# Optimization experiments

Measured on AMD Instinct MI355X. Metric: run time of the kernel, lower is better.

## Reference

```python
import jax, jax.numpy as jnp
import numpy as np

N_NODES = 50000
N_EDGES = 800000
D_FEAT = 100


def setup_inputs() -> dict:
    key = jax.random.key(0)
    ks = jax.random.split(key, 10)
    s = 0.1
    x = jax.random.normal(ks[0], (N_NODES, D_FEAT), dtype=jnp.float32)
    edge_index = jax.random.randint(ks[1], (2, N_EDGES), 0, N_NODES, dtype=jnp.int32)
    return {
        "x": x,
        "edge_index": edge_index,
        "convW0": jax.random.normal(ks[2], (100, 100), jnp.float32) * s,
        "convb0": jnp.zeros((100,), jnp.float32),
        "convW1": jax.random.normal(ks[3], (100, 100), jnp.float32) * s,
        "convb1": jnp.zeros((100,), jnp.float32),
        "linW0": jax.random.normal(ks[4], (100, 10), jnp.float32) * s,
        "linb0": jnp.zeros((10,), jnp.float32),
        "linW1": jax.random.normal(ks[5], (10, 1), jnp.float32) * s,
        "linb1": jnp.zeros((1,), jnp.float32),
    }


def _gcn_conv(x, W, b, src, dst, n):
    """PyG GCNConv: h = x @ W; out[i] = sum_{(j->i)} d_j^{-1/2} d_i^{-1/2} h[j] + b,
    with self-loops already included in (src, dst)."""
    h = x @ W  # [N, out]
    deg = jax.ops.segment_sum(jnp.ones(src.shape[0], x.dtype), dst, num_segments=n)
    dinv = jnp.where(deg > 0, jax.lax.rsqrt(deg), jnp.zeros_like(deg))
    norm = dinv[src] * dinv[dst]  # [E_tot]
    msg = norm[:, None] * h[src]  # gather [E_tot, out]
    out = jax.ops.segment_sum(msg, dst, num_segments=n)  # scatter-add
    return out + b


def reference(x, edge_index, convW0, convb0, convW1, convb1, linW0, linb0, linW1, linb1):
    n = x.shape[0]
    # global-norm division (x.div(torch.norm(x).detach()))
    nm = jax.lax.stop_gradient(jnp.linalg.norm(x))
    x = x / nm
    # NOTE: original re-assigns x via sklearn SelectKBest(chi2, k=100) on raw data.x;
    # that is non-differentiable data preprocessing, so we assume x already holds the
    # k=100 selected features.
    loops = jnp.arange(n, dtype=edge_index.dtype)
    src = jnp.concatenate([edge_index[0], loops])  # self-loops appended
    dst = jnp.concatenate([edge_index[1], loops])
    x = _gcn_conv(x, convW0, convb0, src, dst, n)
    x = _gcn_conv(x, convW1, convb1, src, dst, n)
    # MLP head: ReLU between layers, no activation after the last (loop breaks)
    x = jax.nn.relu(x @ linW0 + linb0)
    x = x @ linW1 + linb1
    return x.T  # [1, N]
```

## Files before the change

### kernel.cpp

```cpp
#include <hip/hip_runtime.h>

#define NN 50000
#define DF 100
#define NE 800000

__device__ __forceinline__ int xcc_id() {
    int x;
    asm volatile("s_getreg_b32 %0, hwreg(HW_REG_XCC_ID)" : "=s"(x));
    return x & 7;
}

__device__ __forceinline__ float wredf(float v) {
    #pragma unroll
    for (int o = 32; o > 0; o >>= 1) v += __shfl_down(v, o, 64);
    return v;
}

__global__ __launch_bounds__(256) void k_pre(const float* __restrict__ x,
                                             float* __restrict__ acc,
                                             const int* __restrict__ src,
                                             const int* __restrict__ dst,
                                             int* __restrict__ cur,
                                             int* __restrict__ ell,
                                             const float* __restrict__ W0,
                                             const float* __restrict__ W1,
                                             const float* __restrict__ cb0,
                                             const float* __restrict__ cb1,
                                             const float* __restrict__ L0,
                                             const float* __restrict__ lb0,
                                             float* __restrict__ Wz,
                                             float* __restrict__ uvec,
                                             float* __restrict__ cvec) {
    int b = blockIdx.x, t = threadIdx.x;
    if (b < 3125) {
        int e = b * 256 + t;
        int d = dst[e];
        int g = xcc_id();
        int p = __hip_atomic_fetch_add(&cur[g * NN + d], 1, __ATOMIC_RELAXED,
                                       __HIP_MEMORY_SCOPE_WORKGROUP);
        if (p < 16) ell[d * 128 + g * 16 + p] = src[e];
    } else if (b < 4149) {
        const float4* x4 = (const float4*)x;
        const int n4 = NN * DF / 4;
        int tid = (b - 3125) * 256 + t, stride = 1024 * 256;
        float s = 0.f;
        for (int i = tid; i < n4; i += stride) {
            float4 v = x4[i];
            s += v.x * v.x + v.y * v.y + v.z * v.z + v.w * v.w;
        }
        s = wredf(s);
        __shared__ float p[4];
        int lane = t & 63, w = t >> 6;
        if (lane == 0) p[w] = s;
        __syncthreads();
        if (t == 0) atomicAdd(acc, p[0] + p[1] + p[2] + p[3]);
    } else {
        __shared__ float WA[1000];
        for (int o = t; o < 1000; o += 256) {
            int j = o / 10, m = o % 10;
            float s = 0.f;
            for (int k = 0; k < 100; ++k) s += W1[j * 100 + k] * L0[k * 10 + m];
            WA[o] = s;
        }
        __syncthreads();
        for (int o = t; o < 1000; o += 256) {
            int i = o / 10, m = o % 10;
            float s = 0.f;
            for (int k = 0; k < 100; ++k) s += W0[i * 100 + k] * WA[k * 10 + m];
            Wz[o] = s;
        }
        if (t < 10) {
            float su = 0.f, scv = 0.f;
            for (int k = 0; k < 100; ++k) {
                su  += cb0[k] * WA[k * 10 + t];
                scv += cb1[k] * L0[k * 10 + t];
            }
            uvec[t] = su;
            cvec[t] = scv + lb0[t];
        }
    }
}

__global__ __launch_bounds__(256) void k_ygemm(const float* __restrict__ x,
                                               const float* __restrict__ Wz,
                                               const int* __restrict__ cur,
                                               int* __restrict__ ell,
                                               int* __restrict__ cnt4A,
                                               float* __restrict__ dinvA,
                                               float* __restrict__ gp) {
    __shared__ float w[1000];
    for (int o = threadIdx.x; o < 1000; o += 256) w[o] = Wz[o];
    __syncthreads();
    int i = blockIdx.x * 256 + threadIdx.x;
    if (i > NN) return;
    if (i == NN) {
        float4 z = {0.f, 0.f, 0.f, 0.f};
        float4* d4 = (float4*)(gp + NN * 16);
        d4[0] = z; d4[1] = z; d4[2] = z; d4[3] = z;
        return;
    }
    int* rp = ell + i * 128;
    int c0 = min(cur[i], 16);
    int total = c0;
    int wpos = c0;
    for (int r = 1; r < 8; ++r) {
        int cr = min(cur[r * NN + i], 16);
        total += cr;
        for (int j = 0; j < cr; ++j) rp[wpos + j] = rp[r * 16 + j];
        wpos += cr;
    }
    int cnt4 = (total + 3) & ~3;
    for (int j = total; j < cnt4; ++j) rp[j] = NN;
    cnt4A[i] = cnt4;
    float dv = rsqrtf((float)(total + 1));
    dinvA[i] = dv;

    const float4* r4 = (const float4*)(x + i * 100);
    float h[10];
    #pragma unroll
    for (int m = 0; m < 10; ++m) h[m] = 0.f;
    for (int kk = 0; kk < 25; ++kk) {
        float4 a = r4[kk];
        #pragma unroll
        for (int j = 0; j < 4; ++j) {
            float av = ((const float*)&a)[j];
            int k = kk * 4 + j;
            #pragma unroll
            for (int m = 0; m < 10; ++m) h[m] += av * w[k * 10 + m];
        }
    }
    float o16[16];
    #pragma unroll
    for (int m = 0; m < 10; ++m) o16[m] = dv * h[m];
    o16[10] = dv;
    o16[11] = o16[12] = o16[13] = o16[14] = o16[15] = 0.f;
    float4* dst4 = (float4*)(gp + i * 16);
    #pragma unroll
    for (int q = 0; q < 4; ++q) dst4[q] = *(float4*)&o16[q * 4];
}

__global__ __launch_bounds__(256) void k_agg1(const float* __restrict__ gp,
                                              const int* __restrict__ cnt4A,
                                              const float* __restrict__ dinvA,
                                              const int* __restrict__ ell,
                                              const float* __restrict__ sumsq,
                                              float* __restrict__ tb) {
    int n = (blockIdx.x * 256 + threadIdx.x) >> 6;
    int l = threadIdx.x & 63;
    int g = l >> 4, lane16 = l & 15;
    if (n > NN) return;
    if (n == NN) {
        if (l < 16) tb[NN * 16 + lane16] = 0.f;
        return;
    }
    int cnt4 = cnt4A[n];
    const int* rp = ell + n * 128;
    float a0 = (g == 0) ? gp[n * 16 + lane16] : 0.f;
    float a1 = 0.f, a2 = 0.f, a3 = 0.f;
    int J = cnt4 >> 2, k = g;
    for (; J >= 4; J -= 4, k += 16) {
        int i0 = rp[k], i1 = rp[k + 4], i2 = rp[k + 8], i3 = rp[k + 12];
        a0 += gp[i0 * 16 + lane16];
        a1 += gp[i1 * 16 + lane16];
        a2 += gp[i2 * 16 + lane16];
        a3 += gp[i3 * 16 + lane16];
    }
    for (; J > 0; --J, k += 4) a0 += gp[rp[k] * 16 + lane16];
    float acc = (a0 + a1) + (a2 + a3);
    acc += __shfl_xor(acc, 16, 64);
    acc += __shfl_xor(acc, 32, 64);
    if (l < 16) {
        float dv = dinvA[n];
        float sc = rsqrtf(*sumsq);
        float o = (lane16 < 10) ? sc * dv * dv * acc
                                : (lane16 == 10 ? dv * acc : 0.f);
        tb[n * 16 + lane16] = o;
    }
}

__global__ __launch_bounds__(256) void k_agg2(const float* __restrict__ tb,
                                              const int* __restrict__ cnt4A,
                                              const float* __restrict__ dinvA,
                                              const int* __restrict__ ell,
                                              const float* __restrict__ u,
                                              const float* __restrict__ cvec,
                                              const float* __restrict__ L1,
                                              const float* __restrict__ lb1,
                                              float* __restrict__ out) {
    __shared__ float su[10], scv[10], sl[10];
    if (threadIdx.x < 10) {
        su[threadIdx.x] = u[threadIdx.x];
        scv[threadIdx.x] = cvec[threadIdx.x];
        sl[threadIdx.x] = L1[threadIdx.x];
    }
    __syncthreads();
    int n = (blockIdx.x * 256 + threadIdx.x) >> 6;
    int l = threadIdx.x & 63;
    int g = l >> 4, lane16 = l & 15;
    int cnt4 = cnt4A[n];
    const int* rp = ell + n * 128;
    float a0 = (g == 0) ? tb[n * 16 + lane16] : 0.f;
    float a1 = 0.f, a2 = 0.f, a3 = 0.f;
    int J = cnt4 >> 2, k = g;
    for (; J >= 4; J -= 4, k += 16) {
        int i0 = rp[k], i1 = rp[k + 4], i2 = rp[k + 8], i3 = rp[k + 12];
        a0 += tb[i0 * 16 + lane16];
        a1 += tb[i1 * 16 + lane16];
        a2 += tb[i2 * 16 + lane16];
        a3 += tb[i3 * 16 + lane16];
    }
    for (; J > 0; --J, k += 4) a0 += tb[rp[k] * 16 + lane16];
    float acc = (a0 + a1) + (a2 + a3);
    acc += __shfl_xor(acc, 16, 64);
    acc += __shfl_xor(acc, 32, 64);
    if (l < 16) {
        float dv = dinvA[n];
        float v = tb[n * 16 + 10];
        float hidden = 0.f;
        if (lane16 < 10)
            hidden = fmaxf(dv * acc + v * su[lane16] + scv[lane16], 0.f) * sl[lane16];
        #pragma unroll
        for (int o = 8; o; o >>= 1) hidden += __shfl_down(hidden, o, 16);
        if (lane16 == 0) out[n] = hidden + lb1[0];
    }
}

extern "C" void kernel_launch(void* const* d_in, const int* in_sizes, int n_in,
                              void* d_out, int out_size, void* d_ws, size_t ws_size,
                              hipStream_t stream) {
    const float* x   = (const float*)d_in[0];
    const int*   ei  = (const int*)d_in[1];
    const int*   src = ei;
    const int*   dst = ei + NE;
    const float* W0  = (const float*)d_in[2];
    const float* cb0 = (const float*)d_in[3];
    const float* W1  = (const float*)d_in[4];
    const float* cb1 = (const float*)d_in[5];
    const float* lw0 = (const float*)d_in[6];
    const float* lb0 = (const float*)d_in[7];
    const float* lw1 = (const float*)d_in[8];
    const float* lb1 = (const float*)d_in[9];
    float* out = (float*)d_out;

    char* ws = (char*)d_ws;
    float* acc     = (float*)(ws + 0);
    int*   cur     = (int*)  (ws + 256);
    const size_t zspan = 1600256;
    float* Wz      = (float*)(ws + 1600512);
    float* uvec    = (float*)(ws + 1604608);
    float* cvec    = (float*)(ws + 1604736);
    int*   ell     = (int*)  (ws + 1604864);
    float* gp      = (float*)(ws + 27204864);
    float* tb      = (float*)(ws + 30404992);
    float* dinvA   = (float*)(ws + 33605120);
    int*   cnt4A   = (int*)  (ws + 33805312);

    hipMemsetAsync(d_ws, 0, zspan, stream);
    k_pre   <<<4150, 256, 0, stream>>>(x, acc, src, dst, cur, ell,
                                       W0, W1, cb0, cb1, lw0, lb0, Wz, uvec, cvec);
    k_ygemm <<<196, 256, 0, stream>>>(x, Wz, cur, ell, cnt4A, dinvA, gp);
    k_agg1  <<<12501, 256, 0, stream>>>(gp, cnt4A, dinvA, ell, acc, tb);
    k_agg2  <<<12500, 256, 0, stream>>>(tb, cnt4A, dinvA, ell, uvec, cvec, lw1, lb1, out);
}
```

Baseline: 211.1 us.

## Fuse ELL build and projection GEMM into one kernel, drop per-XCC bucketing

Merges the preprocessing and projection GEMM kernels into a single launch. Each GEMM block now recomputes the folded weight product itself, and the projection no longer waits on degree counts. The per-XCC 8x16 ELL buckets and compaction pass are replaced by one global atomic cursor per node with a 64-wide ELL, which shrinks the workspace and the memset. Degree normalization moves into aggregation: each neighbor's rsqrt(degree) is computed from the cursor on the fly. That adds an extra cursor gather per edge in layer one, and global atomics may contend more than the former workgroup-scoped ones.

```diff
diff --git a/kernel.cpp b/kernel.cpp
--- a/kernel.cpp
+++ b/kernel.cpp
@@ -3,12 +3,7 @@
 #define NN 50000
 #define DF 100
 #define NE 800000
-
-__device__ __forceinline__ int xcc_id() {
-    int x;
-    asm volatile("s_getreg_b32 %0, hwreg(HW_REG_XCC_ID)" : "=s"(x));
-    return x & 7;
-}
+#define ELLW 64
 
 __device__ __forceinline__ float wredf(float v) {
     #pragma unroll
@@ -16,30 +11,26 @@
     return v;
 }
 
-__global__ __launch_bounds__(256) void k_pre(const float* __restrict__ x,
-                                             float* __restrict__ acc,
-                                             const int* __restrict__ src,
-                                             const int* __restrict__ dst,
-                                             int* __restrict__ cur,
-                                             int* __restrict__ ell,
-                                             const float* __restrict__ W0,
-                                             const float* __restrict__ W1,
-                                             const float* __restrict__ cb0,
-                                             const float* __restrict__ cb1,
-                                             const float* __restrict__ L0,
-                                             const float* __restrict__ lb0,
-                                             float* __restrict__ Wz,
-                                             float* __restrict__ uvec,
-                                             float* __restrict__ cvec) {
+__global__ __launch_bounds__(256) void k_mega(
+    const float* __restrict__ x, float* __restrict__ acc,
+    const int* __restrict__ src, const int* __restrict__ dst,
+    int* __restrict__ cursor, int* __restrict__ ell,
+    const float* __restrict__ W0, const float* __restrict__ W1,
+    const float* __restrict__ cb0, const float* __restrict__ cb1,
+    const float* __restrict__ L0, const float* __restrict__ lb0,
+    float* __restrict__ uvec, float* __restrict__ cvec,
+    float* __restrict__ gp)
+{
     int b = blockIdx.x, t = threadIdx.x;
     if (b < 3125) {
         int e = b * 256 + t;
+        int s = src[e];
         int d = dst[e];
-        int g = xcc_id();
-        int p = __hip_atomic_fetch_add(&cur[g * NN + d], 1, __ATOMIC_RELAXED,
-                                       __HIP_MEMORY_SCOPE_WORKGROUP);
-        if (p < 16) ell[d * 128 + g * 16 + p] = src[e];
-    } else if (b < 4149) {
+        int p = atomicAdd(&cursor[d], 1);
+        if (p < ELLW) ell[d * ELLW + p] = s;
+        return;
+    }
+    if (b < 4149) {
         const float4* x4 = (const float4*)x;
         const int n4 = NN * DF / 4;
         int tid = (b - 3125) * 256 + t, stride = 1024 * 256;
@@ -54,21 +45,17 @@
         if (lane == 0) p[w] = s;
         __syncthreads();
         if (t == 0) atomicAdd(acc, p[0] + p[1] + p[2] + p[3]);
-    } else {
-        __shared__ float WA[1000];
-        for (int o = t; o < 1000; o += 256) {
-            int j = o / 10, m = o % 10;
-            float s = 0.f;
-            for (int k = 0; k < 100; ++k) s += W1[j * 100 + k] * L0[k * 10 + m];
-            WA[o] = s;
-        }
-        __syncthreads();
-        for (int o = t; o < 1000; o += 256) {
-            int i = o / 10, m = o % 10;
-            float s = 0.f;
-            for (int k = 0; k < 100; ++k) s += W0[i * 100 + k] * WA[k * 10 + m];
-            Wz[o] = s;
-        }
+        return;
+    }
+    __shared__ float WA[1000];
+    for (int o = t; o < 1000; o += 256) {
+        int j = o / 10, m = o % 10;
+        float s = 0.f;
+        for (int k = 0; k < 100; ++k) s += W1[j * 100 + k] * L0[k * 10 + m];
+        WA[o] = s;
+    }
+    __syncthreads();
+    if (b == 4345) {
         if (t < 10) {
             float su = 0.f, scv = 0.f;
             for (int k = 0; k < 100; ++k) {
@@ -78,147 +65,137 @@
             uvec[t] = su;
             cvec[t] = scv + lb0[t];
         }
-    }
-}
-
-__global__ __launch_bounds__(256) void k_ygemm(const float* __restrict__ x,
-                                               const float* __restrict__ Wz,
-                                               const int* __restrict__ cur,
-                                               int* __restrict__ ell,
-                                               int* __restrict__ cnt4A,
-                                               float* __restrict__ dinvA,
-                                               float* __restrict__ gp) {
-    __shared__ float w[1000];
-    for (int o = threadIdx.x; o < 1000; o += 256) w[o] = Wz[o];
+        return;
+    }
+    __shared__ float wz[1000];
+    for (int o = t; o < 1000; o += 256) {
+        int i = o / 10, m = o % 10;
+        float s = 0.f;
+        for (int k = 0; k < 100; ++k) s += W0[i * 100 + k] * WA[k * 10 + m];
+        wz[o] = s;
+    }
     __syncthreads();
-    int i = blockIdx.x * 256 + threadIdx.x;
-    if (i > NN) return;
-    if (i == NN) {
+    int i = (b - 4149) * 256 + t;
+    if (i < NN) {
+        const float4* r4 = (const float4*)(x + i * 100);
+        float h[10];
+        #pragma unroll
+        for (int m = 0; m < 10; ++m) h[m] = 0.f;
+        for (int kk = 0; kk < 25; ++kk) {
+            float4 a = r4[kk];
+            #pragma unroll
+            for (int j = 0; j < 4; ++j) {
+                float av = ((const float*)&a)[j];
+                int k = kk * 4 + j;
+                #pragma unroll
+                for (int m = 0; m < 10; ++m) h[m] += av * wz[k * 10 + m];
+            }
+        }
+        float o16[16];
+        #pragma unroll
+        for (int m = 0; m < 10; ++m) o16[m] = h[m];
+        o16[10] = 1.0f;
+        o16[11] = o16[12] = o16[13] = o16[14] = o16[15] = 0.f;
+        float4* dst4 = (float4*)(gp + i * 16);
+        #pragma unroll
+        for (int q = 0; q < 4; ++q) dst4[q] = *(float4*)&o16[q * 4];
+    } else if (i == NN) {
         float4 z = {0.f, 0.f, 0.f, 0.f};
         float4* d4 = (float4*)(gp + NN * 16);
         d4[0] = z; d4[1] = z; d4[2] = z; d4[3] = z;
-        return;
-    }
-    int* rp = ell + i * 128;
-    int c0 = min(cur[i], 16);
-    int total = c0;
-    int wpos = c0;
-    for (int r = 1; r < 8; ++r) {
-        int cr = min(cur[r * NN + i], 16);
-        total += cr;
-        for (int j = 0; j < cr; ++j) rp[wpos + j] = rp[r * 16 + j];
-        wpos += cr;
-    }
-    int cnt4 = (total + 3) & ~3;
-    for (int j = total; j < cnt4; ++j) rp[j] = NN;
-    cnt4A[i] = cnt4;
-    float dv = rsqrtf((float)(total + 1));
-    dinvA[i] = dv;
-
-    const float4* r4 = (const float4*)(x + i * 100);
-    float h[10];
-    #pragma unroll
-    for (int m = 0; m < 10; ++m) h[m] = 0.f;
-    for (int kk = 0; kk < 25; ++kk) {
-        float4 a = r4[kk];
-        #pragma unroll
-        for (int j = 0; j < 4; ++j) {
-            float av = ((const float*)&a)[j];
-            int k = kk * 4 + j;
-            #pragma unroll
-            for (int m = 0; m < 10; ++m) h[m] += av * w[k * 10 + m];
-        }
-    }
-    float o16[16];
-    #pragma unroll
-    for (int m = 0; m < 10; ++m) o16[m] = dv * h[m];
-    o16[10] = dv;
-    o16[11] = o16[12] = o16[13] = o16[14] = o16[15] = 0.f;
-    float4* dst4 = (float4*)(gp + i * 16);
-    #pragma unroll
-    for (int q = 0; q < 4; ++q) dst4[q] = *(float4*)&o16[q * 4];
-}
-
-__global__ __launch_bounds__(256) void k_agg1(const float* __restrict__ gp,
-                                              const int* __restrict__ cnt4A,
-                                              const float* __restrict__ dinvA,
-                                              const int* __restrict__ ell,
-                                              const float* __restrict__ sumsq,
-                                              float* __restrict__ tb) {
+    }
+}
+
+__global__ __launch_bounds__(256) void k_agg1(
+    const float* __restrict__ gp, const int* __restrict__ cursor,
+    const int* __restrict__ ell, const float* __restrict__ acc,
+    float* __restrict__ tb)
+{
     int n = (blockIdx.x * 256 + threadIdx.x) >> 6;
-    int l = threadIdx.x & 63;
-    int g = l >> 4, lane16 = l & 15;
+    int l = threadIdx.x & 63, g = l >> 4, lane16 = l & 15;
     if (n > NN) return;
     if (n == NN) {
         if (l < 16) tb[NN * 16 + lane16] = 0.f;
         return;
     }
-    int cnt4 = cnt4A[n];
-    const int* rp = ell + n * 128;
-    float a0 = (g == 0) ? gp[n * 16 + lane16] : 0.f;
+    int deg = cursor[n];
+    int lim = min(deg, ELLW);
+    float dvn = rsqrtf((float)(deg + 1));
+    const int* rp = ell + n * ELLW;
+    float a0 = (g == 0) ? dvn * gp[n * 16 + lane16] : 0.f;
     float a1 = 0.f, a2 = 0.f, a3 = 0.f;
-    int J = cnt4 >> 2, k = g;
-    for (; J >= 4; J -= 4, k += 16) {
-        int i0 = rp[k], i1 = rp[k + 4], i2 = rp[k + 8], i3 = rp[k + 12];
-        a0 += gp[i0 * 16 + lane16];
-        a1 += gp[i1 * 16 + lane16];
-        a2 += gp[i2 * 16 + lane16];
-        a3 += gp[i3 * 16 + lane16];
-    }
-    for (; J > 0; --J, k += 4) a0 += gp[rp[k] * 16 + lane16];
-    float acc = (a0 + a1) + (a2 + a3);
-    acc += __shfl_xor(acc, 16, 64);
-    acc += __shfl_xor(acc, 32, 64);
+    int nq = (lim + 3) >> 2;
+    int k = g, q = 0;
+    for (; q + 4 <= nq; q += 4, k += 16) {
+        int i0 = (k      < lim) ? rp[k]      : NN;
+        int i1 = (k + 4  < lim) ? rp[k + 4]  : NN;
+        int i2 = (k + 8  < lim) ? rp[k + 8]  : NN;
+        int i3 = (k + 12 < lim) ? rp[k + 12] : NN;
+        a0 += rsqrtf((float)(cursor[i0] + 1)) * gp[i0 * 16 + lane16];
+        a1 += rsqrtf((float)(cursor[i1] + 1)) * gp[i1 * 16 + lane16];
+        a2 += rsqrtf((float)(cursor[i2] + 1)) * gp[i2 * 16 + lane16];
+        a3 += rsqrtf((float)(cursor[i3] + 1)) * gp[i3 * 16 + lane16];
+    }
+    for (; q < nq; ++q, k += 4) {
+        int i0 = (k < lim) ? rp[k] : NN;
+        a0 += rsqrtf((float)(cursor[i0] + 1)) * gp[i0 * 16 + lane16];
+    }
+    float s = (a0 + a1) + (a2 + a3);
+    s += __shfl_xor(s, 16, 64);
+    s += __shfl_xor(s, 32, 64);
     if (l < 16) {
-        float dv = dinvA[n];
-        float sc = rsqrtf(*sumsq);
-        float o = (lane16 < 10) ? sc * dv * dv * acc
-                                : (lane16 == 10 ? dv * acc : 0.f);
+        float sc = rsqrtf(*acc);
+        float o = (lane16 < 10) ? sc * dvn * dvn * s
+                                : (lane16 == 10 ? dvn * s : 0.f);
         tb[n * 16 + lane16] = o;
     }
 }
 
-__global__ __launch_bounds__(256) void k_agg2(const float* __restrict__ tb,
-                                              const int* __restrict__ cnt4A,
-                                              const float* __restrict__ dinvA,
-                                              const int* __restrict__ ell,
-                                              const float* __restrict__ u,
-                                              const float* __restrict__ cvec,
-                                              const float* __restrict__ L1,
-                                              const float* __restrict__ lb1,
-                                              float* __restrict__ out) {
+__global__ __launch_bounds__(256) void k_agg2(
+    const float* __restrict__ tb, const int* __restrict__ cursor,
+    const int* __restrict__ ell, const float* __restrict__ uvec,
+    const float* __restrict__ cvec, const float* __restrict__ L1,
+    const float* __restrict__ lb1, float* __restrict__ out)
+{
     __shared__ float su[10], scv[10], sl[10];
     if (threadIdx.x < 10) {
-        su[threadIdx.x] = u[threadIdx.x];
+        su[threadIdx.x]  = uvec[threadIdx.x];
         scv[threadIdx.x] = cvec[threadIdx.x];
-        sl[threadIdx.x] = L1[threadIdx.x];
+        sl[threadIdx.x]  = L1[threadIdx.x];
     }
     __syncthreads();
     int n = (blockIdx.x * 256 + threadIdx.x) >> 6;
-    int l = threadIdx.x & 63;
-    int g = l >> 4, lane16 = l & 15;
-    int cnt4 = cnt4A[n];
-    const int* rp = ell + n * 128;
+    int l = threadIdx.x & 63, g = l >> 4, lane16 = l & 15;
+    int deg = cursor[n];
+    int lim = min(deg, ELLW);
+    float dvn = rsqrtf((float)(deg + 1));
+    const int* rp = ell + n * ELLW;
     float a0 = (g == 0) ? tb[n * 16 + lane16] : 0.f;
     float a1 = 0.f, a2 = 0.f, a3 = 0.f;
-    int J = cnt4 >> 2, k = g;
-    for (; J >= 4; J -= 4, k += 16) {
-        int i0 = rp[k], i1 = rp[k + 4], i2 = rp[k + 8], i3 = rp[k + 12];
+    int nq = (lim + 3) >> 2;
+    int k = g, q = 0;
+    for (; q + 4 <= nq; q += 4, k += 16) {
+        int i0 = (k      < lim) ? rp[k]      : NN;
+        int i1 = (k + 4  < lim) ? rp[k + 4]  : NN;
+        int i2 = (k + 8  < lim) ? rp[k + 8]  : NN;
+        int i3 = (k + 12 < lim) ? rp[k + 12] : NN;
         a0 += tb[i0 * 16 + lane16];
         a1 += tb[i1 * 16 + lane16];
         a2 += tb[i2 * 16 + lane16];
         a3 += tb[i3 * 16 + lane16];
     }
-    for (; J > 0; --J, k += 4) a0 += tb[rp[k] * 16 + lane16];
-    float acc = (a0 + a1) + (a2 + a3);
-    acc += __shfl_xor(acc, 16, 64);
-    acc += __shfl_xor(acc, 32, 64);
+    for (; q < nq; ++q, k += 4) {
+        int i0 = (k < lim) ? rp[k] : NN;
+        a0 += tb[i0 * 16 + lane16];
+    }
+    float s = (a0 + a1) + (a2 + a3);
+    s += __shfl_xor(s, 16, 64);
+    s += __shfl_xor(s, 32, 64);
     if (l < 16) {
-        float dv = dinvA[n];
         float v = tb[n * 16 + 10];
         float hidden = 0.f;
         if (lane16 < 10)
-            hidden = fmaxf(dv * acc + v * su[lane16] + scv[lane16], 0.f) * sl[lane16];
+            hidden = fmaxf(dvn * s + v * su[lane16] + scv[lane16], 0.f) * sl[lane16];
         #pragma unroll
         for (int o = 8; o; o >>= 1) hidden += __shfl_down(hidden, o, 16);
         if (lane16 == 0) out[n] = hidden + lb1[0];
@@ -244,21 +221,17 @@
 
     char* ws = (char*)d_ws;
     float* acc     = (float*)(ws + 0);
-    int*   cur     = (int*)  (ws + 256);
-    const size_t zspan = 1600256;
-    float* Wz      = (float*)(ws + 1600512);
-    float* uvec    = (float*)(ws + 1604608);
-    float* cvec    = (float*)(ws + 1604736);
-    int*   ell     = (int*)  (ws + 1604864);
-    float* gp      = (float*)(ws + 27204864);
-    float* tb      = (float*)(ws + 30404992);
-    float* dinvA   = (float*)(ws + 33605120);
-    int*   cnt4A   = (int*)  (ws + 33805312);
+    int*   cursor  = (int*)  (ws + 256);
+    const size_t zspan = 200320;
+    float* uvec    = (float*)(ws + 200320);
+    float* cvec    = (float*)(ws + 200448);
+    int*   ell     = (int*)  (ws + 200704);
+    float* gp      = (float*)(ws + 13000704);
+    float* tb      = (float*)(ws + 16200768);
 
     hipMemsetAsync(d_ws, 0, zspan, stream);
-    k_pre   <<<4150, 256, 0, stream>>>(x, acc, src, dst, cur, ell,
-                                       W0, W1, cb0, cb1, lw0, lb0, Wz, uvec, cvec);
-    k_ygemm <<<196, 256, 0, stream>>>(x, Wz, cur, ell, cnt4A, dinvA, gp);
-    k_agg1  <<<12501, 256, 0, stream>>>(gp, cnt4A, dinvA, ell, acc, tb);
-    k_agg2  <<<12500, 256, 0, stream>>>(tb, cnt4A, dinvA, ell, uvec, cvec, lw1, lb1, out);
-}
+    k_mega <<<4346, 256, 0, stream>>>(x, acc, src, dst, cursor, ell,
+                                      W0, W1, cb0, cb1, lw0, lb0, uvec, cvec, gp);
+    k_agg1 <<<12501, 256, 0, stream>>>(gp, cursor, ell, acc, tb);
+    k_agg2 <<<12500, 256, 0, stream>>>(tb, cursor, ell, uvec, cvec, lw1, lb1, out);
+}
```

New measurement: 244.0 us. 1.16x slower.
